# Optimization experiments

Hardware: AMD Instinct MI355X
Metric: run time of the kernel (lower is better)

Reference implementation:

```python
import jax, jax.numpy as jnp
import numpy as np


def setup_inputs() -> dict:
    key = jax.random.key(0)
    k1, k2, k3 = jax.random.split(key, 3)
    B, T, J, D = 32, 2048, 512, 256
    context = jax.random.normal(k1, (B, T, D), dtype=jnp.float32)
    question = jax.random.normal(k2, (B, J, D), dtype=jnp.float32)
    kernel = jax.random.normal(k3, (3 * D, 1), dtype=jnp.float32) * 0.05
    return {"context": context, "question": question, "kernel": kernel}


def reference(context, question, kernel):
    # Original: tile context to (B,T,J,d), question to (B,T,J,d), concat with
    # elementwise product -> (B,T,J,3d), dot with kernel (3d,1), squeeze.
    # Algebraically identical decomposition (kernel = [wc; wq; wm]):
    #   S[b,t,j] = c[b,t]@wc + q[b,j]@wq + (c[b,t]*wm)@q[b,j]
    D = context.shape[-1]
    w = jnp.squeeze(kernel, axis=-1)          # (3d,)
    wc, wq, wm = w[:D], w[D:2 * D], w[2 * D:]
    c_term = context @ wc                     # (B, T)
    q_term = question @ wq                    # (B, J)
    cross = jnp.einsum('btd,bjd->btj', context * wm, question)  # (B, T, J)
    return cross + c_term[:, :, None] + q_term[:, None, :]
```

## Files before the change

### kernel.cpp

```cpp
#include <hip/hip_runtime.h>
#include <stdint.h>

typedef __bf16 bf16x8 __attribute__((ext_vector_type(8)));
typedef float  f32x4  __attribute__((ext_vector_type(4)));

typedef __attribute__((address_space(1))) const void g_void;
typedef __attribute__((address_space(3))) void l_void;

constexpr int NB = 32, TT = 2048, JJ = 512, DD = 256;
constexpr int CTX_ROWS = NB * TT;
constexpr int QUE_ROWS = NB * JJ;
constexpr int ALL_ROWS = CTX_ROWS + QUE_ROWS;

constexpr size_t WS_QUEB  = 33554432;
constexpr size_t WS_CTERM = 41943040;
constexpr size_t WS_QTERM = 42205184;
constexpr size_t WS_NEED  = 42270720;

__global__ __launch_bounds__(256)
void prep_kernel(const float* __restrict__ ctx, const float* __restrict__ que,
                 const float* __restrict__ wvec,
                 __bf16* __restrict__ ctxb, __bf16* __restrict__ queb,
                 float* __restrict__ cterm, float* __restrict__ qterm)
{
    const int tid  = threadIdx.x;
    const int colg = tid & 31;
    const int rloc = tid >> 5;
    const int k0   = colg * 8;

    const f32x4 wc0 = *(const f32x4*)(wvec + k0);
    const f32x4 wc1 = *(const f32x4*)(wvec + k0 + 4);
    const f32x4 wq0 = *(const f32x4*)(wvec + DD + k0);
    const f32x4 wq1 = *(const f32x4*)(wvec + DD + k0 + 4);
    const f32x4 wm0 = *(const f32x4*)(wvec + 2 * DD + k0);
    const f32x4 wm1 = *(const f32x4*)(wvec + 2 * DD + k0 + 4);

    for (int r = blockIdx.x * 8 + rloc; r < ALL_ROWS; r += gridDim.x * 8) {
        const bool isC = (r < CTX_ROWS);
        const int  rr  = isC ? r : (r - CTX_ROWS);
        const float* src = (isC ? ctx : que) + (size_t)rr * DD + k0;
        const f32x4 x0 = *(const f32x4*)src;
        const f32x4 x1 = *(const f32x4*)(src + 4);

        const f32x4 wd0 = isC ? wc0 : wq0;
        const f32x4 wd1 = isC ? wc1 : wq1;
        float d = x0[0]*wd0[0] + x0[1]*wd0[1] + x0[2]*wd0[2] + x0[3]*wd0[3]
                + x1[0]*wd1[0] + x1[1]*wd1[1] + x1[2]*wd1[2] + x1[3]*wd1[3];
        d += __shfl_xor(d, 1);  d += __shfl_xor(d, 2);  d += __shfl_xor(d, 4);
        d += __shfl_xor(d, 8);  d += __shfl_xor(d, 16);

        bf16x8 pk;
        #pragma unroll
        for (int j = 0; j < 4; ++j) {
            pk[j]     = (__bf16)(isC ? x0[j] * wm0[j] : x0[j]);
            pk[4 + j] = (__bf16)(isC ? x1[j] * wm1[j] : x1[j]);
        }
        *(bf16x8*)((isC ? ctxb : queb) + (size_t)rr * DD + k0) = pk;
        if (colg == 0) (isC ? cterm : qterm)[rr] = d;
    }
}

__global__ __launch_bounds__(256)
void gemm_kernel(const __bf16* __restrict__ ctxb, const __bf16* __restrict__ queb,
                 const float* __restrict__ cterm, const float* __restrict__ qterm,
                 float* __restrict__ out)
{
    __shared__ __align__(1024) unsigned char lds[32768];

    const int tid = threadIdx.x;
    const int l   = tid & 63;
    const int wid = tid >> 6;

    const int pb = blockIdx.x;
    const int id = (pb & 7) * 256 + (pb >> 3);
    const int n0 = (id & 3) * 128;
    const int m0 = ((id >> 2) & 15) * 128;
    const int bI = id >> 6;

    const int lrow8 = l >> 3;
    const int lslot = l & 7;
    const int srcsw = (lslot ^ lrow8) << 3;

    const __bf16* aBase = ctxb + ((size_t)bI * TT + m0 + wid * 32 + lrow8) * DD + srcsw;
    const __bf16* bBase = queb + ((size_t)bI * JJ + n0 + wid * 32 + lrow8) * DD + srcsw;
    unsigned char* ldsA = lds + wid * 4096;
    unsigned char* ldsB = lds + 16384 + wid * 4096;

    auto stage = [&](int k) {
        #pragma unroll
        for (int j = 0; j < 4; ++j) {
            __builtin_amdgcn_global_load_lds((g_void*)(aBase + (size_t)j * 8 * DD + k * 64),
                                             (l_void*)(ldsA + j * 1024), 16, 0, 0);
            __builtin_amdgcn_global_load_lds((g_void*)(bBase + (size_t)j * 8 * DD + k * 64),
                                             (l_void*)(ldsB + j * 1024), 16, 0, 0);
        }
    };

    stage(0);

    f32x4 acc[4][4];
    #pragma unroll
    for (int m = 0; m < 4; ++m)
        #pragma unroll
        for (int n = 0; n < 4; ++n) acc[m][n] = f32x4{0.f, 0.f, 0.f, 0.f};

    const int wm_0 = (wid >> 1) * 64;
    const int wn_0 = (wid & 1) * 64;
    const int lr = l & 15;
    const int hi = l >> 4;

    #pragma unroll
    for (int k = 0; k < 4; ++k) {
        asm volatile("s_waitcnt vmcnt(0)" ::: "memory");
        __builtin_amdgcn_s_barrier();

        bf16x8 af[2][4], bfr[2][4];
        #pragma unroll
        for (int kk = 0; kk < 2; ++kk) {
            const int c = kk * 4 + hi;
            #pragma unroll
            for (int m = 0; m < 4; ++m) {
                const int r = wm_0 + m * 16 + lr;
                af[kk][m] = *(const bf16x8*)(lds + r * 128 + ((c ^ (r & 7)) << 4));
            }
            #pragma unroll
            for (int n = 0; n < 4; ++n) {
                const int r = wn_0 + n * 16 + lr;
                bfr[kk][n] = *(const bf16x8*)(lds + 16384 + r * 128 + ((c ^ (r & 7)) << 4));
            }
        }
        asm volatile("s_waitcnt lgkmcnt(0)" ::: "memory");
        __builtin_amdgcn_sched_barrier(0);
        __builtin_amdgcn_s_barrier();
        if (k < 3) stage(k + 1);

        __builtin_amdgcn_s_setprio(1);
        #pragma unroll
        for (int kk = 0; kk < 2; ++kk)
            #pragma unroll
            for (int m = 0; m < 4; ++m)
                #pragma unroll
                for (int n = 0; n < 4; ++n)
                    acc[m][n] = __builtin_amdgcn_mfma_f32_16x16x32_bf16(af[kk][m], bfr[kk][n],
                                                                        acc[m][n], 0, 0, 0);
        __builtin_amdgcn_s_setprio(0);
    }

    const int lq = hi * 4;
    #pragma unroll
    for (int m = 0; m < 4; ++m) {
        const int rowL = wm_0 + m * 16 + lq;
        const f32x4 cv = *(const f32x4*)(cterm + (size_t)bI * TT + m0 + rowL);
        #pragma unroll
        for (int n = 0; n < 4; ++n) {
            const int colL = wn_0 + n * 16 + lr;
            const float qv = qterm[(size_t)bI * JJ + n0 + colL];
            float* dst = out + ((size_t)bI * TT + m0 + rowL) * JJ + (n0 + colL);
            const f32x4 v = acc[m][n];
            #pragma unroll
            for (int q = 0; q < 4; ++q)
                dst[(size_t)q * JJ] = v[q] + cv[q] + qv;
        }
    }
}

__global__ __launch_bounds__(256)
void naive_kernel(const float* __restrict__ ctx, const float* __restrict__ que,
                  const float* __restrict__ wvec, float* __restrict__ out)
{
    const int j = blockIdx.x * 16 + (threadIdx.x & 15);
    const int t = blockIdx.y * 16 + (threadIdx.x >> 4);
    const int b = blockIdx.z;
    const float* cr = ctx + ((size_t)b * TT + t) * DD;
    const float* qr = que + ((size_t)b * JJ + j) * DD;
    float s = 0.f, ct = 0.f, qt = 0.f;
    for (int k = 0; k < DD; ++k) {
        const float cv = cr[k], qv = qr[k];
        s  += cv * wvec[2 * DD + k] * qv;
        ct += cv * wvec[k];
        qt += qv * wvec[DD + k];
    }
    out[((size_t)b * TT + t) * JJ + j] = s + ct + qt;
}

extern "C" void kernel_launch(void* const* d_in, const int* in_sizes, int n_in,
                              void* d_out, int out_size, void* d_ws, size_t ws_size,
                              hipStream_t stream) {
    (void)in_sizes; (void)n_in; (void)out_size;
    const float* ctx = (const float*)d_in[0];
    const float* que = (const float*)d_in[1];
    const float* wv  = (const float*)d_in[2];
    float* out = (float*)d_out;

    if (ws_size < WS_NEED) {
        naive_kernel<<<dim3(JJ / 16, TT / 16, NB), dim3(256), 0, stream>>>(ctx, que, wv, out);
        return;
    }

    __bf16* ctxb = (__bf16*)d_ws;
    __bf16* queb = (__bf16*)((char*)d_ws + WS_QUEB);
    float*  cterm = (float*)((char*)d_ws + WS_CTERM);
    float*  qterm = (float*)((char*)d_ws + WS_QTERM);

    prep_kernel<<<dim3(2048), dim3(256), 0, stream>>>(ctx, que, wv, ctxb, queb, cterm, qterm);
    gemm_kernel<<<dim3(2048), dim3(256), 0, stream>>>(ctxb, queb, cterm, qterm, out);
}
```

Before: 56.55 us.

## Swap MFMA operands for row-contiguous vector nontemporal stores; split prep blocks

The GEMM swaps the A/B operands of the MFMA so each lane's accumulator holds 4 consecutive output columns. The epilogue can then write float4 nontemporal stores instead of 4 scalar stores strided by a row. The prep kernel gives context and question rows their own block ranges (2560 blocks). This removes per-row branching and the select between weight vectors. The output writes are the dominant traffic, so wider coalesced stores are the main intent.

```diff
diff --git a/kernel.cpp b/kernel.cpp
--- a/kernel.cpp
+++ b/kernel.cpp
@@ -10,7 +10,6 @@
 constexpr int NB = 32, TT = 2048, JJ = 512, DD = 256;
 constexpr int CTX_ROWS = NB * TT;
 constexpr int QUE_ROWS = NB * JJ;
-constexpr int ALL_ROWS = CTX_ROWS + QUE_ROWS;
 
 constexpr size_t WS_QUEB  = 33554432;
 constexpr size_t WS_CTERM = 41943040;
@@ -28,22 +27,25 @@
     const int rloc = tid >> 5;
     const int k0   = colg * 8;
 
-    const f32x4 wc0 = *(const f32x4*)(wvec + k0);
-    const f32x4 wc1 = *(const f32x4*)(wvec + k0 + 4);
-    const f32x4 wq0 = *(const f32x4*)(wvec + DD + k0);
-    const f32x4 wq1 = *(const f32x4*)(wvec + DD + k0 + 4);
-    const f32x4 wm0 = *(const f32x4*)(wvec + 2 * DD + k0);
-    const f32x4 wm1 = *(const f32x4*)(wvec + 2 * DD + k0 + 4);
-
-    for (int r = blockIdx.x * 8 + rloc; r < ALL_ROWS; r += gridDim.x * 8) {
-        const bool isC = (r < CTX_ROWS);
-        const int  rr  = isC ? r : (r - CTX_ROWS);
-        const float* src = (isC ? ctx : que) + (size_t)rr * DD + k0;
+    const bool isC = (blockIdx.x < 2048);
+    const float* src0  = isC ? ctx  : que;
+    __bf16*      dst0  = isC ? ctxb : queb;
+    float*       term0 = isC ? cterm : qterm;
+    const int    rows   = isC ? CTX_ROWS : QUE_ROWS;
+    const int    stride = isC ? 2048 * 8 : 512 * 8;
+    const int    rg0    = isC ? blockIdx.x : blockIdx.x - 2048;
+
+    const f32x4 wd0 = *(const f32x4*)(wvec + (isC ? 0 : DD) + k0);
+    const f32x4 wd1 = *(const f32x4*)(wvec + (isC ? 0 : DD) + k0 + 4);
+    f32x4 wm0 = {1.f, 1.f, 1.f, 1.f}, wm1 = {1.f, 1.f, 1.f, 1.f};
+    if (isC) { wm0 = *(const f32x4*)(wvec + 2 * DD + k0);
+               wm1 = *(const f32x4*)(wvec + 2 * DD + k0 + 4); }
+
+    for (int r = rg0 * 8 + rloc; r < rows; r += stride) {
+        const float* src = src0 + (size_t)r * DD + k0;
         const f32x4 x0 = *(const f32x4*)src;
         const f32x4 x1 = *(const f32x4*)(src + 4);
 
-        const f32x4 wd0 = isC ? wc0 : wq0;
-        const f32x4 wd1 = isC ? wc1 : wq1;
         float d = x0[0]*wd0[0] + x0[1]*wd0[1] + x0[2]*wd0[2] + x0[3]*wd0[3]
                 + x1[0]*wd1[0] + x1[1]*wd1[1] + x1[2]*wd1[2] + x1[3]*wd1[3];
         d += __shfl_xor(d, 1);  d += __shfl_xor(d, 2);  d += __shfl_xor(d, 4);
@@ -52,11 +54,11 @@
         bf16x8 pk;
         #pragma unroll
         for (int j = 0; j < 4; ++j) {
-            pk[j]     = (__bf16)(isC ? x0[j] * wm0[j] : x0[j]);
-            pk[4 + j] = (__bf16)(isC ? x1[j] * wm1[j] : x1[j]);
-        }
-        *(bf16x8*)((isC ? ctxb : queb) + (size_t)rr * DD + k0) = pk;
-        if (colg == 0) (isC ? cterm : qterm)[rr] = d;
+            pk[j]     = (__bf16)(x0[j] * wm0[j]);
+            pk[4 + j] = (__bf16)(x1[j] * wm1[j]);
+        }
+        *(bf16x8*)(dst0 + (size_t)r * DD + k0) = pk;
+        if (colg == 0) term0[r] = d;
     }
 }
 
@@ -141,25 +143,25 @@
             for (int m = 0; m < 4; ++m)
                 #pragma unroll
                 for (int n = 0; n < 4; ++n)
-                    acc[m][n] = __builtin_amdgcn_mfma_f32_16x16x32_bf16(af[kk][m], bfr[kk][n],
+                    acc[m][n] = __builtin_amdgcn_mfma_f32_16x16x32_bf16(bfr[kk][n], af[kk][m],
                                                                         acc[m][n], 0, 0, 0);
         __builtin_amdgcn_s_setprio(0);
     }
 
-    const int lq = hi * 4;
+    const int jb = wn_0 + hi * 4;
     #pragma unroll
     for (int m = 0; m < 4; ++m) {
-        const int rowL = wm_0 + m * 16 + lq;
-        const f32x4 cv = *(const f32x4*)(cterm + (size_t)bI * TT + m0 + rowL);
+        const int rowL = wm_0 + m * 16 + lr;
+        const float cv = cterm[(size_t)bI * TT + m0 + rowL];
+        float* rowp = out + ((size_t)bI * TT + m0 + rowL) * JJ + n0;
         #pragma unroll
         for (int n = 0; n < 4; ++n) {
-            const int colL = wn_0 + n * 16 + lr;
-            const float qv = qterm[(size_t)bI * JJ + n0 + colL];
-            float* dst = out + ((size_t)bI * TT + m0 + rowL) * JJ + (n0 + colL);
+            const int colL = jb + n * 16;
+            const f32x4 qv = *(const f32x4*)(qterm + (size_t)bI * JJ + n0 + colL);
             const f32x4 v = acc[m][n];
-            #pragma unroll
-            for (int q = 0; q < 4; ++q)
-                dst[(size_t)q * JJ] = v[q] + cv[q] + qv;
+            f32x4 w = {v[0] + cv + qv[0], v[1] + cv + qv[1],
+                       v[2] + cv + qv[2], v[3] + cv + qv[3]};
+            __builtin_nontemporal_store(w, (f32x4*)(rowp + colL));
         }
     }
 }
@@ -202,6 +204,6 @@
     float*  cterm = (float*)((char*)d_ws + WS_CTERM);
     float*  qterm = (float*)((char*)d_ws + WS_QTERM);
 
-    prep_kernel<<<dim3(2048), dim3(256), 0, stream>>>(ctx, que, wv, ctxb, queb, cterm, qterm);
+    prep_kernel<<<dim3(2560), dim3(256), 0, stream>>>(ctx, que, wv, ctxb, queb, cterm, qterm);
     gemm_kernel<<<dim3(2048), dim3(256), 0, stream>>>(ctxb, queb, cterm, qterm, out);
 }
```

Result: slower. 71.02 us (+25.6%).

## Drop LDS staging; each wave computes independent 64x64 tile from global loads

Applied to the files above, without the earlier changes.

The GEMM kernel no longer stages A/B tiles through shared memory with async global-to-LDS copies and barriers. Each wave now owns its own 64x64 output tile and loads MFMA fragments directly from global memory across the full K dimension. MFMA operands are swapped so each lane holds four consecutive output columns, which allows 16-byte vector stores with vectorized qterm loads. This removes barriers and LDS traffic but also removes operand reuse across waves, raising L2/global load traffic, and the loads now have no explicit prefetch overlap.

```diff
diff --git a/kernel.cpp b/kernel.cpp
--- a/kernel.cpp
+++ b/kernel.cpp
@@ -3,9 +3,6 @@
 
 typedef __bf16 bf16x8 __attribute__((ext_vector_type(8)));
 typedef float  f32x4  __attribute__((ext_vector_type(4)));
-
-typedef __attribute__((address_space(1))) const void g_void;
-typedef __attribute__((address_space(3))) void l_void;
 
 constexpr int NB = 32, TT = 2048, JJ = 512, DD = 256;
 constexpr int CTX_ROWS = NB * TT;
@@ -65,38 +62,22 @@
                  const float* __restrict__ cterm, const float* __restrict__ qterm,
                  float* __restrict__ out)
 {
-    __shared__ __align__(1024) unsigned char lds[32768];
-
-    const int tid = threadIdx.x;
-    const int l   = tid & 63;
-    const int wid = tid >> 6;
+    const int l   = threadIdx.x & 63;
+    const int w   = threadIdx.x >> 6;
 
     const int pb = blockIdx.x;
     const int id = (pb & 7) * 256 + (pb >> 3);
-    const int n0 = (id & 3) * 128;
-    const int m0 = ((id >> 2) & 15) * 128;
-    const int bI = id >> 6;
 
-    const int lrow8 = l >> 3;
-    const int lslot = l & 7;
-    const int srcsw = (lslot ^ lrow8) << 3;
+    const int tile = id * 4 + w;
+    const int n0 = (tile & 7) * 64;
+    const int m0 = ((tile >> 3) & 31) * 64;
+    const int bI = tile >> 8;
 
-    const __bf16* aBase = ctxb + ((size_t)bI * TT + m0 + wid * 32 + lrow8) * DD + srcsw;
-    const __bf16* bBase = queb + ((size_t)bI * JJ + n0 + wid * 32 + lrow8) * DD + srcsw;
-    unsigned char* ldsA = lds + wid * 4096;
-    unsigned char* ldsB = lds + 16384 + wid * 4096;
+    const int lr = l & 15;
+    const int hi = l >> 4;
 
-    auto stage = [&](int k) {
-        #pragma unroll
-        for (int j = 0; j < 4; ++j) {
-            __builtin_amdgcn_global_load_lds((g_void*)(aBase + (size_t)j * 8 * DD + k * 64),
-                                             (l_void*)(ldsA + j * 1024), 16, 0, 0);
-            __builtin_amdgcn_global_load_lds((g_void*)(bBase + (size_t)j * 8 * DD + k * 64),
-                                             (l_void*)(ldsB + j * 1024), 16, 0, 0);
-        }
-    };
-
-    stage(0);
+    const __bf16* aB = ctxb + ((size_t)bI * TT + m0 + lr) * DD + hi * 8;
+    const __bf16* bB = queb + ((size_t)bI * JJ + n0 + lr) * DD + hi * 8;
 
     f32x4 acc[4][4];
     #pragma unroll
@@ -104,62 +85,38 @@
         #pragma unroll
         for (int n = 0; n < 4; ++n) acc[m][n] = f32x4{0.f, 0.f, 0.f, 0.f};
 
-    const int wm_0 = (wid >> 1) * 64;
-    const int wn_0 = (wid & 1) * 64;
-    const int lr = l & 15;
-    const int hi = l >> 4;
+    #pragma unroll
+    for (int w8 = 0; w8 < 8; ++w8) {
+        bf16x8 af[4], bfr[4];
+        #pragma unroll
+        for (int m = 0; m < 4; ++m)
+            af[m] = *(const bf16x8*)(aB + (size_t)(m * 16) * DD + w8 * 32);
+        #pragma unroll
+        for (int n = 0; n < 4; ++n)
+            bfr[n] = *(const bf16x8*)(bB + (size_t)(n * 16) * DD + w8 * 32);
 
-    #pragma unroll
-    for (int k = 0; k < 4; ++k) {
-        asm volatile("s_waitcnt vmcnt(0)" ::: "memory");
-        __builtin_amdgcn_s_barrier();
-
-        bf16x8 af[2][4], bfr[2][4];
         #pragma unroll
-        for (int kk = 0; kk < 2; ++kk) {
-            const int c = kk * 4 + hi;
+        for (int m = 0; m < 4; ++m)
             #pragma unroll
-            for (int m = 0; m < 4; ++m) {
-                const int r = wm_0 + m * 16 + lr;
-                af[kk][m] = *(const bf16x8*)(lds + r * 128 + ((c ^ (r & 7)) << 4));
-            }
-            #pragma unroll
-            for (int n = 0; n < 4; ++n) {
-                const int r = wn_0 + n * 16 + lr;
-                bfr[kk][n] = *(const bf16x8*)(lds + 16384 + r * 128 + ((c ^ (r & 7)) << 4));
-            }
-        }
-        asm volatile("s_waitcnt lgkmcnt(0)" ::: "memory");
-        __builtin_amdgcn_sched_barrier(0);
-        __builtin_amdgcn_s_barrier();
-        if (k < 3) stage(k + 1);
-
-        __builtin_amdgcn_s_setprio(1);
-        #pragma unroll
-        for (int kk = 0; kk < 2; ++kk)
-            #pragma unroll
-            for (int m = 0; m < 4; ++m)
-                #pragma unroll
-                for (int n = 0; n < 4; ++n)
-                    acc[m][n] = __builtin_amdgcn_mfma_f32_16x16x32_bf16(af[kk][m], bfr[kk][n],
-                                                                        acc[m][n], 0, 0, 0);
-        __builtin_amdgcn_s_setprio(0);
+            for (int n = 0; n < 4; ++n)
+                acc[m][n] = __builtin_amdgcn_mfma_f32_16x16x32_bf16(bfr[n], af[m],
+                                                                    acc[m][n], 0, 0, 0);
     }
 
-    const int lq = hi * 4;
+    const int jb = hi * 4;
     #pragma unroll
     for (int m = 0; m < 4; ++m) {
-        const int rowL = wm_0 + m * 16 + lq;
-        const f32x4 cv = *(const f32x4*)(cterm + (size_t)bI * TT + m0 + rowL);
+        const int rowG = m0 + m * 16 + lr;
+        const float cv = cterm[(size_t)bI * TT + rowG];
+        float* rowp = out + ((size_t)bI * TT + rowG) * JJ + n0;
         #pragma unroll
         for (int n = 0; n < 4; ++n) {
-            const int colL = wn_0 + n * 16 + lr;
-            const float qv = qterm[(size_t)bI * JJ + n0 + colL];
-            float* dst = out + ((size_t)bI * TT + m0 + rowL) * JJ + (n0 + colL);
+            const int colL = n * 16 + jb;
+            const f32x4 qv = *(const f32x4*)(qterm + (size_t)bI * JJ + n0 + colL);
             const f32x4 v = acc[m][n];
-            #pragma unroll
-            for (int q = 0; q < 4; ++q)
-                dst[(size_t)q * JJ] = v[q] + cv[q] + qv;
+            f32x4 o = {v[0] + cv + qv[0], v[1] + cv + qv[1],
+                       v[2] + cv + qv[2], v[3] + cv + qv[3]};
+            *(f32x4*)(rowp + colL) = o;
         }
     }
 }
```

After: 97.17 us. 71.8% more time.
